# Optimization experiments

Measured on AMD Instinct MI355X. Metric: run time of the kernel, lower is better.

The kernel has to match this reference:

```python
import jax, jax.numpy as jnp
import numpy as np

B, N, D, H, K = 16, 256, 64, 64, 2  # batch, nodes, d_in, d_hidden, top_k


def setup_inputs() -> dict:
    key = jax.random.key(0)
    k0, k1, k2 = jax.random.split(key, 3)
    O = jax.random.normal(k0, (B, N, D), dtype=jnp.float32)
    # PairwiseFeaturizer.proj: Linear(4*D, H) -> ReLU -> Linear(H, 1)
    W1 = jax.random.normal(k1, (4 * D, H), dtype=jnp.float32) / np.sqrt(4 * D).astype(np.float32)
    b1 = jnp.zeros((H,), dtype=jnp.float32)
    W2 = jax.random.normal(k2, (H, 1), dtype=jnp.float32) / np.sqrt(H).astype(np.float32)
    b2 = jnp.zeros((1,), dtype=jnp.float32)
    return {"O": O, "W1": W1, "b1": b1, "W2": W2, "b2": b2}


def reference(O, W1, b1, W2, b2):
    Bn, Nn, d = O.shape
    ii, jj = jnp.triu_indices(Nn, k=1)  # all undirected pairs i<j, M = N(N-1)/2
    Oi = O[:, ii, :]  # (B, M, d) gather
    Oj = O[:, jj, :]  # (B, M, d) gather
    feats = jnp.concatenate([Oi, Oj, jnp.abs(Oi - Oj), Oi * Oj], axis=-1)  # (B, M, 4d)
    h = jax.nn.relu(jnp.einsum('bmf,fh->bmh', feats, W1) + b1)
    Q = (jnp.einsum('bmh,ho->bmo', h, W2) + b2)[..., 0]  # (B, M)
    # greedy top-k selection mask (eps -> 0 limit of select_pairs)
    idx = jax.lax.top_k(Q, K)[1]  # (B, K)
    mask = jnp.zeros(Q.shape, dtype=bool).at[jnp.arange(Q.shape[0])[:, None], idx].set(True)
    return Q, mask
```

## Files before the change

### kernel.cpp

```cpp
#include <hip/hip_runtime.h>
#include <math.h>

#define Bn 16
#define Nn 256
#define Mm (Nn*(Nn-1)/2)
#define CHUNK 4080

typedef __attribute__((ext_vector_type(8))) _Float16 f16x8;
typedef __attribute__((ext_vector_type(4))) _Float16 f16x4;
typedef __attribute__((ext_vector_type(4))) float f32x4;

typedef union { f16x8 v; _Float16 h[8]; unsigned u[4]; } H8;
typedef union { f16x4 v; _Float16 h[4]; } H4;

#define MFMA(acc, a, b) \
  acc = __builtin_amdgcn_mfma_f32_16x16x32_f16((a), (b), (acc), 0, 0, 0)

__device__ __forceinline__ void top2_update(float v, int m,
    float& v1, int& i1, float& v2, int& i2)
{
  bool c1 = (v > v1) || (v == v1 && m < i1);
  bool c2 = (v > v2) || (v == v2 && m < i2);
  float nv2 = c1 ? v1 : (c2 ? v : v2);
  int   ni2 = c1 ? i1 : (c2 ? m : i2);
  v1 = c1 ? v : v1;  i1 = c1 ? m : i1;
  v2 = nv2;          i2 = ni2;
}

__global__ __launch_bounds__(256) void prep_all(
    const float* __restrict__ O, const float* __restrict__ W1,
    const float* __restrict__ b1,
    _Float16* __restrict__ wtg, _Float16* __restrict__ obg,
    float* __restrict__ Ag, _Float16* __restrict__ Cgh)
{
  const int t = threadIdx.x;
  if (blockIdx.x < 64) {
    const int h = blockIdx.x;
    wtg[h * 256 + t] = (_Float16)W1[t * 64 + h];
    return;
  }

  __shared__ __align__(16) _Float16 s_ob[64][72];
  __shared__ __align__(16) _Float16 s_w[64][136];
  const int l = t & 63, wv = t >> 6;
  const int lo = l & 15, g = l >> 4;
  const int bb = blockIdx.x - 64;
  const int b = bb >> 2, rt = bb & 3;
  const int r0 = rt * 64;
  const float* Ob = O + ((size_t)b * Nn + r0) * 64;

  #pragma unroll
  for (int p = 0; p < 4; ++p) {
    int v = t + p * 256;
    int r = v >> 4, c4 = (v & 15) * 4;
    float4 x = ((const float4*)Ob)[v];
    H4 pk; pk.h[0] = (_Float16)x.x; pk.h[1] = (_Float16)x.y;
           pk.h[2] = (_Float16)x.z; pk.h[3] = (_Float16)x.w;
    *(f16x4*)&s_ob[r][c4] = pk.v;
    *(f16x4*)&obg[((size_t)b * Nn + r0 + r) * 64 + c4] = pk.v;
  }
  #pragma unroll
  for (int p = 0; p < 32; ++p) {
    int kk = p * 4 + (t >> 6), h = t & 63;
    s_w[h][kk] = (_Float16)W1[kk * 64 + h];
  }
  __syncthreads();

  H8 aop[2];
  #pragma unroll
  for (int ks = 0; ks < 2; ++ks)
    aop[ks].v = *(const f16x8*)&s_ob[wv * 16 + lo][ks * 32 + g * 8];

  #pragma unroll
  for (int half = 0; half < 2; ++half) {
    #pragma unroll
    for (int nf = 0; nf < 4; ++nf) {
      f32x4 ac = {0.f, 0.f, 0.f, 0.f};
      #pragma unroll
      for (int ks = 0; ks < 2; ++ks) {
        H8 bop; bop.v = *(const f16x8*)&s_w[nf * 16 + lo][half * 64 + ks * 32 + g * 8];
        MFMA(ac, aop[ks].v, bop.v);
      }
      const int h = nf * 16 + lo;
      if (half == 0) {
        float bbv = b1[h];
        #pragma unroll
        for (int r = 0; r < 4; ++r)
          Ag[((size_t)b * Nn + r0 + wv * 16 + g * 4 + r) * 64 + h] = ac[r] + bbv;
      } else {
        #pragma unroll
        for (int r = 0; r < 4; ++r)
          Cgh[((size_t)b * Nn + r0 + wv * 16 + g * 4 + r) * 64 + h] = (_Float16)ac[r];
      }
    }
  }
}

__global__ __launch_bounds__(256, 2) void pair_kernel(
    const _Float16* __restrict__ obg,
    const float* __restrict__ Ag,
    const _Float16* __restrict__ Cgh,
    const float* __restrict__ W2,
    const float* __restrict__ b2,
    const _Float16* __restrict__ wtg,
    float* __restrict__ Q,
    float* __restrict__ cand)
{
  __shared__ __align__(16) _Float16 s_wt[64][136];
  __shared__ float s_w2[64];
  __shared__ float s_red[4][4];

  const int t  = threadIdx.x;
  const int l  = t & 63, wv = t >> 6;
  const int lo = l & 15, g = l >> 4;

  const int blk    = blockIdx.x;
  const int within = blk >> 3;
  const int batch  = (blk & 7) * 2 + within / 72;
  int tl           = within % 72;
  int a = 0;
  while (tl >= 8 - (a >> 1)) { tl -= 8 - (a >> 1); ++a; }
  const int c   = (a >> 1) + tl;
  const int ti0 = a * 16, tj0 = c * 32;
  const bool isdiag = (tj0 < ti0 + 16);

  const size_t obase = (size_t)batch * Nn;
  const size_t qbase = (size_t)batch * Mm;

  {
    const int h = t >> 2, kq = (t & 3) * 32;
    #pragma unroll
    for (int q = 0; q < 4; ++q)
      *(f16x8*)&s_wt[h][kq + q * 8] =
          *(const f16x8*)&wtg[h * 256 + 128 + kq + q * 8];
    if (t < 64) s_w2[t] = W2[t];
  }
  __syncthreads();

  H8 bfr[4][4];
  #pragma unroll
  for (int ks = 0; ks < 4; ++ks)
    #pragma unroll
    for (int nf = 0; nf < 4; ++nf)
      bfr[ks][nf].v = *(const f16x8*)&s_wt[nf * 16 + lo][ks * 32 + g * 8];

  H8 ojb[2][2];
  #pragma unroll
  for (int jh = 0; jh < 2; ++jh) {
    ojb[jh][0].v = *(const f16x8*)&obg[(obase + tj0 + jh * 16 + lo) * 64 + g * 8];
    ojb[jh][1].v = *(const f16x8*)&obg[(obase + tj0 + jh * 16 + lo) * 64 + 32 + g * 8];
  }
  f32x4 cinf[2][4];
  #pragma unroll
  for (int jh = 0; jh < 2; ++jh)
    #pragma unroll
    for (int nf = 0; nf < 4; ++nf) {
      H4 cx; cx.v = *(const f16x4*)
          &Cgh[(obase + tj0 + jh * 16 + lo) * 64 + nf * 16 + g * 4];
      #pragma unroll
      for (int r = 0; r < 4; ++r) cinf[jh][nf][r] = (float)cx.h[r];
    }

  const float b2v = b2[0];

  H8 oib0, oib1;
  f32x4 as4[4];
  int iG = 0, mbG = 0, iP = 0, mbP = 0;
  f32x4 acc0[4], acc1[4];
  H8 f0, f1, f2, f3;
  float v1 = -INFINITY, v2 = -INFINITY;
  int   i1 = 0x7fffffff, i2 = 0x7fffffff;

  auto LOADROW = [&](int ii) {
    const int i = ti0 + wv * 4 + ii;
    oib0.v = *(const f16x8*)&obg[(obase + i) * 64 + g * 8];
    oib1.v = *(const f16x8*)&obg[(obase + i) * 64 + 32 + g * 8];
    #pragma unroll
    for (int nf = 0; nf < 4; ++nf)
      as4[nf] = *(const f32x4*)&Ag[(obase + i) * 64 + nf * 16 + g * 4];
    iG = i;
    mbG = i * (Nn - 1) - (i * (i - 1)) / 2 - i - 1;
  };

  auto BUILD = [&](const H8& oj0, const H8& oj1) {
    H8 d0, d1;
    d0.v = oib0.v - oj0.v;
    d1.v = oib1.v - oj1.v;
    #pragma unroll
    for (int q = 0; q < 4; ++q) {
      d0.u[q] &= 0x7FFF7FFFu;
      d1.u[q] &= 0x7FFF7FFFu;
    }
    f0 = d0; f1 = d1;
    f2.v = oib0.v * oj0.v;
    f3.v = oib1.v * oj1.v;
  };

  auto STEP = [&](f32x4 (&acc)[4]) {
    #pragma unroll
    for (int nf = 0; nf < 4; ++nf) acc[nf] = as4[nf];
    MFMA(acc[0], bfr[0][0].v, f0.v); MFMA(acc[1], bfr[0][1].v, f0.v);
    MFMA(acc[2], bfr[0][2].v, f0.v); MFMA(acc[3], bfr[0][3].v, f0.v);
    MFMA(acc[0], bfr[1][0].v, f1.v); MFMA(acc[1], bfr[1][1].v, f1.v);
    MFMA(acc[2], bfr[1][2].v, f1.v); MFMA(acc[3], bfr[1][3].v, f1.v);
    MFMA(acc[0], bfr[2][0].v, f2.v); MFMA(acc[1], bfr[2][1].v, f2.v);
    MFMA(acc[2], bfr[2][2].v, f2.v); MFMA(acc[3], bfr[2][3].v, f2.v);
    MFMA(acc[0], bfr[3][0].v, f3.v); MFMA(acc[1], bfr[3][1].v, f3.v);
    MFMA(acc[2], bfr[3][2].v, f3.v); MFMA(acc[3], bfr[3][3].v, f3.v);
  };

  auto EPI = [&](f32x4 (&acc)[4], int jhE, int iE, int mbE) {
    float part = 0.f;
    #pragma unroll
    for (int nf = 0; nf < 4; ++nf) {
      f32x4 w2v = *(const f32x4*)&s_w2[nf * 16 + g * 4];
      #pragma unroll
      for (int r = 0; r < 4; ++r) {
        float z = acc[nf][r] + cinf[jhE][nf][r];
        part = fmaf(fmaxf(z, 0.f), w2v[r], part);
      }
    }
    part += __shfl_xor(part, 16);
    part += __shfl_xor(part, 32);
    if (l < 16) {
      const int j = tj0 + jhE * 16 + l;
      if (!isdiag || j > iE) {
        const float qv = part + b2v;
        const int m = mbE + j;
        Q[qbase + m] = qv;
        top2_update(qv, m, v1, i1, v2, i2);
      }
    }
  };

  LOADROW(0);
  BUILD(ojb[0][0], ojb[0][1]); STEP(acc0);
  BUILD(ojb[1][0], ojb[1][1]); STEP(acc1); EPI(acc0, 0, iG, mbG);

  iP = iG; mbP = mbG; LOADROW(1);
  EPI(acc1, 1, iP, mbP);
  BUILD(ojb[0][0], ojb[0][1]); STEP(acc0);
  BUILD(ojb[1][0], ojb[1][1]); STEP(acc1); EPI(acc0, 0, iG, mbG);

  iP = iG; mbP = mbG; LOADROW(2);
  EPI(acc1, 1, iP, mbP);
  BUILD(ojb[0][0], ojb[0][1]); STEP(acc0);
  BUILD(ojb[1][0], ojb[1][1]); STEP(acc1); EPI(acc0, 0, iG, mbG);

  iP = iG; mbP = mbG; LOADROW(3);
  EPI(acc1, 1, iP, mbP);
  BUILD(ojb[0][0], ojb[0][1]); STEP(acc0);
  BUILD(ojb[1][0], ojb[1][1]); STEP(acc1); EPI(acc0, 0, iG, mbG);
  EPI(acc1, 1, iG, mbG);

  #pragma unroll
  for (int s = 1; s < 64; s <<= 1) {
    float u1 = __shfl_xor(v1, s); int j1 = __shfl_xor(i1, s);
    float u2 = __shfl_xor(v2, s); int j2 = __shfl_xor(i2, s);
    top2_update(u1, j1, v1, i1, v2, i2);
    top2_update(u2, j2, v1, i1, v2, i2);
  }
  if (l == 0) {
    s_red[wv][0] = v1; s_red[wv][1] = __int_as_float(i1);
    s_red[wv][2] = v2; s_red[wv][3] = __int_as_float(i2);
  }
  __syncthreads();
  if (t == 0) {
    float a1 = s_red[0][0]; int x1 = __float_as_int(s_red[0][1]);
    float a2 = s_red[0][2]; int x2 = __float_as_int(s_red[0][3]);
    #pragma unroll
    for (int e = 1; e < 4; ++e) {
      top2_update(s_red[e][0], __float_as_int(s_red[e][1]), a1, x1, a2, x2);
      top2_update(s_red[e][2], __float_as_int(s_red[e][3]), a1, x1, a2, x2);
    }
    float* cp = cand + ((size_t)batch * 72 + within % 72) * 4;
    cp[0] = a1; cp[1] = __int_as_float(x1);
    cp[2] = a2; cp[3] = __int_as_float(x2);
  }
}

__global__ __launch_bounds__(256) void rankmask_kernel(
    const float* __restrict__ O, const float* __restrict__ W1,
    const float* __restrict__ b1, const float* __restrict__ W2,
    const float* __restrict__ cand, float* __restrict__ mask)
{
  const int b   = blockIdx.x >> 3;
  const int cch = blockIdx.x & 7;
  const int t   = threadIdx.x;
  const int wv  = t >> 6, h = t & 63;
  __shared__ float s_cv[144];
  __shared__ int   s_ci[144];
  __shared__ int   s_m[8];
  __shared__ int   s_ij[8][2];
  __shared__ float s_or[8][2][64];
  __shared__ float s_qe[8];
  __shared__ int   s_k0, s_k1;

  if (t < 144) {
    const float* cp = cand + (size_t)(b * 72 + (t >> 1)) * 4;
    s_cv[t] = cp[(t & 1) * 2];
    s_ci[t] = __float_as_int(cp[(t & 1) * 2 + 1]);
  }
  __syncthreads();
  if (t < 144) {
    float v = s_cv[t]; int m = s_ci[t];
    int rank = 0;
    for (int e = 0; e < 144; ++e) {
      float u = s_cv[e]; int n = s_ci[e];
      rank += (u > v || (u == v && n < m)) ? 1 : 0;
    }
    if (rank < 8) s_m[rank] = m;
  }
  __syncthreads();
  if (t < 16) {
    int m = s_m[t >> 1];
    int i = 0, rem = m;
    while (rem >= Nn - 1 - i) { rem -= Nn - 1 - i; ++i; }
    int j = i + 1 + rem;
    s_ij[t >> 1][t & 1] = (t & 1) ? j : i;
  }
  __syncthreads();
  {
    int cc = t >> 5, rr = (t >> 4) & 1, c4 = (t & 15) * 4;
    int row = s_ij[cc][rr];
    *(float4*)&s_or[cc][rr][c4] = *(const float4*)&O[((size_t)b * Nn + row) * 64 + c4];
  }
  __syncthreads();
  #pragma unroll
  for (int p = 0; p < 2; ++p) {
    const int cc = p * 4 + wv;
    float z = b1[h];
    #pragma unroll 8
    for (int d = 0; d < 64; ++d) {
      float oi = s_or[cc][0][d], oj = s_or[cc][1][d];
      float f3 = fabsf(oi - oj), f4 = oi * oj;
      z += oi * W1[d * 64 + h] + oj * W1[(64 + d) * 64 + h]
         + f3 * W1[(128 + d) * 64 + h] + f4 * W1[(192 + d) * 64 + h];
    }
    float part = fmaxf(z, 0.f) * W2[h];
    #pragma unroll
    for (int s = 1; s < 64; s <<= 1) part += __shfl_xor(part, s);
    if (h == 0) s_qe[cc] = part;
  }
  __syncthreads();
  if (t == 0) {
    float v1 = -INFINITY, v2 = -INFINITY;
    int   i1 = 0x7fffffff, i2 = 0x7fffffff;
    for (int e = 0; e < 8; ++e)
      top2_update(s_qe[e], s_m[e], v1, i1, v2, i2);
    s_k0 = i1; s_k1 = i2;
  }
  __syncthreads();

  const int k0 = s_k0, k1 = s_k1;
  float* mb = mask + (size_t)b * Mm;
  const int m0 = cch * CHUNK;
  for (int m = m0 + t; m < m0 + CHUNK; m += 256)
    mb[m] = (m == k0 || m == k1) ? 1.0f : 0.0f;
}

extern "C" void kernel_launch(void* const* d_in, const int* in_sizes, int n_in,
                              void* d_out, int out_size, void* d_ws, size_t ws_size,
                              hipStream_t stream) {
  const float* O  = (const float*)d_in[0];
  const float* W1 = (const float*)d_in[1];
  const float* b1 = (const float*)d_in[2];
  const float* W2 = (const float*)d_in[3];
  const float* b2 = (const float*)d_in[4];

  float* Q    = (float*)d_out;
  float* mask = Q + (size_t)Bn * Mm;

  char* ws = (char*)d_ws;
  _Float16* wtg = (_Float16*)ws;
  _Float16* obg = (_Float16*)(ws + 32768);
  float*    Ag  = (float*)(ws + 32768 + 524288);
  _Float16* Cgh = (_Float16*)(ws + 32768 + 524288 + 1048576);
  float*    cand = (float*)(ws + 32768 + 524288 + 1048576 + 524288);

  prep_all<<<dim3(128), dim3(256), 0, stream>>>(O, W1, b1, wtg, obg, Ag, Cgh);
  pair_kernel<<<dim3(Bn * 72), dim3(256), 0, stream>>>(obg, Ag, Cgh, W2, b2, wtg, Q, cand);
  rankmask_kernel<<<dim3(Bn * 8), dim3(256), 0, stream>>>(O, W1, b1, W2, cand, mask);
}
```

Baseline: 58.36 us.

## Cut register pressure in pair_kernel to raise occupancy to four blocks per CU

Raises the launch-bounds minimum blocks per CU from 2 to 4 for pair_kernel. To make that fit, the W1 fragments are no longer held in registers but reloaded from LDS inside each MFMA step, and the C-term is kept as packed fp16 and converted inside the epilogue. W2 is preloaded into registers and the epilogue reduction is split into four independent FMA chains. The aim is more waves to hide latency, at the cost of extra LDS reads per MFMA group and possible spills if the register cap is too tight.

```diff
diff --git a/kernel.cpp b/kernel.cpp
--- a/kernel.cpp
+++ b/kernel.cpp
@@ -96,7 +96,7 @@
   }
 }
 
-__global__ __launch_bounds__(256, 2) void pair_kernel(
+__global__ __launch_bounds__(256, 4) void pair_kernel(
     const _Float16* __restrict__ obg,
     const float* __restrict__ Ag,
     const _Float16* __restrict__ Cgh,
@@ -137,29 +137,23 @@
   }
   __syncthreads();
 
-  H8 bfr[4][4];
-  #pragma unroll
-  for (int ks = 0; ks < 4; ++ks)
-    #pragma unroll
-    for (int nf = 0; nf < 4; ++nf)
-      bfr[ks][nf].v = *(const f16x8*)&s_wt[nf * 16 + lo][ks * 32 + g * 8];
-
   H8 ojb[2][2];
   #pragma unroll
   for (int jh = 0; jh < 2; ++jh) {
     ojb[jh][0].v = *(const f16x8*)&obg[(obase + tj0 + jh * 16 + lo) * 64 + g * 8];
     ojb[jh][1].v = *(const f16x8*)&obg[(obase + tj0 + jh * 16 + lo) * 64 + 32 + g * 8];
   }
-  f32x4 cinf[2][4];
+  H4 cinb[2][4];
   #pragma unroll
   for (int jh = 0; jh < 2; ++jh)
     #pragma unroll
-    for (int nf = 0; nf < 4; ++nf) {
-      H4 cx; cx.v = *(const f16x4*)
+    for (int nf = 0; nf < 4; ++nf)
+      cinb[jh][nf].v = *(const f16x4*)
           &Cgh[(obase + tj0 + jh * 16 + lo) * 64 + nf * 16 + g * 4];
-      #pragma unroll
-      for (int r = 0; r < 4; ++r) cinf[jh][nf][r] = (float)cx.h[r];
-    }
+  f32x4 w2r[4];
+  #pragma unroll
+  for (int nf = 0; nf < 4; ++nf)
+    w2r[nf] = *(const f32x4*)&s_w2[nf * 16 + g * 4];
 
   const float b2v = b2[0];
 
@@ -199,27 +193,32 @@
   auto STEP = [&](f32x4 (&acc)[4]) {
     #pragma unroll
     for (int nf = 0; nf < 4; ++nf) acc[nf] = as4[nf];
-    MFMA(acc[0], bfr[0][0].v, f0.v); MFMA(acc[1], bfr[0][1].v, f0.v);
-    MFMA(acc[2], bfr[0][2].v, f0.v); MFMA(acc[3], bfr[0][3].v, f0.v);
-    MFMA(acc[0], bfr[1][0].v, f1.v); MFMA(acc[1], bfr[1][1].v, f1.v);
-    MFMA(acc[2], bfr[1][2].v, f1.v); MFMA(acc[3], bfr[1][3].v, f1.v);
-    MFMA(acc[0], bfr[2][0].v, f2.v); MFMA(acc[1], bfr[2][1].v, f2.v);
-    MFMA(acc[2], bfr[2][2].v, f2.v); MFMA(acc[3], bfr[2][3].v, f2.v);
-    MFMA(acc[0], bfr[3][0].v, f3.v); MFMA(acc[1], bfr[3][1].v, f3.v);
-    MFMA(acc[2], bfr[3][2].v, f3.v); MFMA(acc[3], bfr[3][3].v, f3.v);
+    #pragma unroll
+    for (int ks = 0; ks < 4; ++ks) {
+      H8 w0, w1, w2q, w3;
+      w0.v  = *(const f16x8*)&s_wt[       lo][ks * 32 + g * 8];
+      w1.v  = *(const f16x8*)&s_wt[16  + lo][ks * 32 + g * 8];
+      w2q.v = *(const f16x8*)&s_wt[32  + lo][ks * 32 + g * 8];
+      w3.v  = *(const f16x8*)&s_wt[48  + lo][ks * 32 + g * 8];
+      const f16x8 fk = (ks == 0) ? f0.v : (ks == 1) ? f1.v
+                     : (ks == 2) ? f2.v : f3.v;
+      MFMA(acc[0], w0.v,  fk);
+      MFMA(acc[1], w1.v,  fk);
+      MFMA(acc[2], w2q.v, fk);
+      MFMA(acc[3], w3.v,  fk);
+    }
   };
 
   auto EPI = [&](f32x4 (&acc)[4], int jhE, int iE, int mbE) {
-    float part = 0.f;
-    #pragma unroll
-    for (int nf = 0; nf < 4; ++nf) {
-      f32x4 w2v = *(const f32x4*)&s_w2[nf * 16 + g * 4];
-      #pragma unroll
-      for (int r = 0; r < 4; ++r) {
-        float z = acc[nf][r] + cinf[jhE][nf][r];
-        part = fmaf(fmaxf(z, 0.f), w2v[r], part);
-      }
-    }
+    float p0 = 0.f, p1 = 0.f, p2 = 0.f, p3 = 0.f;
+    #pragma unroll
+    for (int r = 0; r < 4; ++r) {
+      p0 = fmaf(fmaxf(acc[0][r] + (float)cinb[jhE][0].h[r], 0.f), w2r[0][r], p0);
+      p1 = fmaf(fmaxf(acc[1][r] + (float)cinb[jhE][1].h[r], 0.f), w2r[1][r], p1);
+      p2 = fmaf(fmaxf(acc[2][r] + (float)cinb[jhE][2].h[r], 0.f), w2r[2][r], p2);
+      p3 = fmaf(fmaxf(acc[3][r] + (float)cinb[jhE][3].h[r], 0.f), w2r[3][r], p3);
+    }
+    float part = (p0 + p1) + (p2 + p3);
     part += __shfl_xor(part, 16);
     part += __shfl_xor(part, 32);
     if (l < 16) {
```

Measured after the change: 89.07 us. +52.6%, slower.
